# Performance work log

Measured on AMD Instinct MI355X. Metric: run time of the kernel, lower is better.

## Reference

```python
import jax, jax.numpy as jnp
import numpy as np

B, C, H, W = 8, 64, 256, 256
N_HEADS = 4
MODES_X, MODES_Y = 32, 32 // 2 + 1  # rfft half-spectrum along last dim
O_PER_HEAD = C // N_HEADS


def setup_inputs() -> dict:
    key = jax.random.key(0)
    k1, k2, k3 = jax.random.split(key, 3)
    x = jax.random.normal(k1, (B, C, H, W), dtype=jnp.float32)
    weights_real = jax.random.normal(k2, (N_HEADS, C, O_PER_HEAD, MODES_X, MODES_Y), dtype=jnp.float32) * 0.01
    weights_imag = jax.random.normal(k3, (N_HEADS, C, O_PER_HEAD, MODES_X, MODES_Y), dtype=jnp.float32) * 0.01
    bias = jnp.zeros((C, 1, 1), dtype=jnp.float32)
    return {"x": x, "weights_real": weights_real, "weights_imag": weights_imag, "bias": bias}


def reference(x, weights_real, weights_imag, bias):
    b, c, h, w = x.shape
    nh, _, o, mxw, myw = weights_real.shape
    # rfft2 with ortho norm, matching torch.fft.rfft2(..., norm='ortho')
    xf = jnp.fft.rfft2(x, norm="ortho")  # [B, C, H, W//2+1] complex64
    fH, fW = xf.shape[-2], xf.shape[-1]
    mx = min(mxw, fH)
    my = min(myw, fW)
    wgt = weights_real[..., :mx, :my] + 1j * weights_imag[..., :mx, :my]  # [nh, C, o, mx, my]
    # all heads at once: torch loop 'biXY,ioXY->boXY' per head == 'bixy,hioxy->bhoxy'
    prod = jnp.einsum("bixy,hioxy->bhoxy", xf[:, :, :mx, :my], wgt)  # [B, nh, o, mx, my]
    out_f = jnp.zeros((b, nh, o, fH, fW), dtype=prod.dtype).at[..., :mx, :my].set(prod)
    out = jnp.fft.irfft2(out_f, s=(h, w), norm="ortho")  # [B, nh, o, H, W] real
    # torch.cat over heads along channel dim == head-major reshape
    out = out.reshape(b, nh * o, h, w)
    return out + bias  # bias [C,1,1] broadcasts
```

## Files before the change

kernel.cpp:

```cpp
#include <hip/hip_runtime.h>
#include <hip/hip_bf16.h>

#define NROWS 131072
#define MY 17
#define MX 32


#define K1_ROWS 30
#define NCHUNK 9

__global__ __launch_bounds__(512) void f1_fw(const float* __restrict__ x,
                                             float2* __restrict__ X2) {
    __shared__ __align__(16) float s_lds[4][K1_ROWS][68];
    __shared__ float2 xs[4352];
    int t = threadIdx.x;
    int bc = blockIdx.x;
    const float* xp = x + (long)bc * 65536;

    int j = t % 17;
    int r = t / 17;
    int rc = r < K1_ROWS ? r : 0;
    int odd = j & 1;
    float ca = odd ? 0.f : ((j & 2) ? -1.f : 1.f);
    float cb = odd ? (((j & 3) == 1) ? -1.f : 1.f) : 0.f;
    float cj, sj;
    sincospif((float)j * (1.0f / 128.0f), &sj, &cj);
    sj = -sj;
    float swv, cwv;
    sincospif((float)j * 0.25f, &swv, &cwv);
    swv = -swv;
    float k1c = cwv * ca - swv * cb;
    float k2c = swv * ca + cwv * cb;
    const float4* A4 = (const float4*)&s_lds[odd ? 1 : 0][rc][0];
    const float4* B4 = (const float4*)&s_lds[odd ? 3 : 2][rc][0];

    float4 q0, q1, q2, q3;

#define F1_REGLOAD(cc)                                                         \
    {                                                                          \
        int nr_ = ((cc) < 8) ? K1_ROWS : 16;                                   \
        int items_ = nr_ * 16;                                                 \
        int it = t < items_ ? t : items_ - 1;                                  \
        int rr = it >> 4, cq = it & 15;                                        \
        const float4* xr =                                                     \
            (const float4*)(xp + ((cc) * K1_ROWS + rr) * 256) + cq;            \
        q0 = xr[0];                                                            \
        q1 = xr[16];                                                           \
        q2 = xr[32];                                                           \
        q3 = xr[48];                                                           \
    }

    F1_REGLOAD(0)

    for (int c = 0; c < NCHUNK; ++c) {
        int nr = (c < 8) ? K1_ROWS : 16;
        int items = nr * 16;

        if (t < items) {
            int rr = t >> 4, cq = t & 15;
            float4 s02p, s02m, s13p, s13m;
            s02p.x = q0.x + q2.x; s02p.y = q0.y + q2.y;
            s02p.z = q0.z + q2.z; s02p.w = q0.w + q2.w;
            s02m.x = q0.x - q2.x; s02m.y = q0.y - q2.y;
            s02m.z = q0.z - q2.z; s02m.w = q0.w - q2.w;
            s13p.x = q1.x + q3.x; s13p.y = q1.y + q3.y;
            s13p.z = q1.z + q3.z; s13p.w = q1.w + q3.w;
            s13m.x = q1.x - q3.x; s13m.y = q1.y - q3.y;
            s13m.z = q1.z - q3.z; s13m.w = q1.w - q3.w;
            *(float4*)&s_lds[0][rr][cq * 4] = s02p;
            *(float4*)&s_lds[1][rr][cq * 4] = s02m;
            *(float4*)&s_lds[2][rr][cq * 4] = s13p;
            *(float4*)&s_lds[3][rr][cq * 4] = s13m;
        }
        __syncthreads();

        if (c + 1 < NCHUNK) F1_REGLOAD(c + 1)

        if (t < 510 && r < nr) {
            float pc = 1.f, ps = 0.f;
            float ar0 = 0, ai0 = 0;

#define K1_STEP(a0e, b0e, a0f, b0f)                                   \
  { float t0re = fmaf(k1c, (b0f), fmaf(cwv, (a0f), fmaf(ca, (b0e), (a0e)))); \
    float t0im = fmaf(k2c, (b0f), fmaf(swv, (a0f), cb * (b0e)));      \
    ar0 = fmaf(t0re, pc, ar0); ar0 = fmaf(-t0im, ps, ar0);            \
    ai0 = fmaf(t0re, ps, ai0); ai0 = fmaf(t0im, pc, ai0);             \
    float nps = fmaf(pc, sj, ps * cj);                                \
    pc = fmaf(pc, cj, -(ps * sj)); ps = nps; }

#pragma unroll 2
            for (int l4 = 0; l4 < 8; ++l4) {
                float4 va0 = A4[l4], vb0 = B4[l4];
                float4 vA0 = A4[8 + l4], vB0 = B4[8 + l4];
                K1_STEP(va0.x, vb0.x, vA0.x, vB0.x)
                K1_STEP(va0.y, vb0.y, vA0.y, vB0.y)
                K1_STEP(va0.z, vb0.z, vA0.z, vB0.z)
                K1_STEP(va0.w, vb0.w, vA0.w, vB0.w)
            }
#undef K1_STEP

            int h = c * K1_ROWS + r;
            xs[h * 17 + j] = make_float2(ar0, ai0);
        }
        __syncthreads();
    }

    for (int q = t; q < 2176; q += 512) {
        float2 a = xs[q], b = xs[q + 2176];
        xs[q] = make_float2(a.x + b.x, a.y + b.y);
        xs[q + 2176] = make_float2(a.x - b.x, a.y - b.y);
    }
    __syncthreads();

    for (int q = t; q < 544; q += 512) {
        int kx = q / 17, ky = q % 17;
        int kodd = kx & 1;
        float cA = kodd ? 0.f : ((kx & 2) ? -1.f : 1.f);
        float cB = kodd ? (((kx & 3) == 1) ? -1.f : 1.f) : 0.f;
        float cBn = -cB;
        const float2* Aq = xs + (kodd ? 2176 : 0) + ky;
        float cs, ss;
        sincospif((float)kx * (1.0f / 128.0f), &ss, &cs);
        ss = -ss;
        float pc = 1.f, psn = 0.f;
        float ar = 0.f, ai = 0.f;
#pragma unroll 4
        for (int m = 0; m < 64; ++m) {
            float2 a = Aq[m * 17];
            float2 b = Aq[1088 + m * 17];
            float yre = fmaf(cBn, b.y, fmaf(cA, b.x, a.x));
            float yim = fmaf(cB, b.x, fmaf(cA, b.y, a.y));
            ar = fmaf(yre, pc, ar); ar = fmaf(-yim, psn, ar);
            ai = fmaf(yre, psn, ai); ai = fmaf(yim, pc, ai);
            float npc = pc * cs - psn * ss;
            psn = pc * ss + psn * cs;
            pc = npc;
        }
        X2[(long)bc * 544 + q] = make_float2(ar, ai);
    }
#undef F1_REGLOAD
}

__global__ __launch_bounds__(512) void k_ab(const float2* __restrict__ X2,
                                            const float* __restrict__ wr_g,
                                            const float* __restrict__ wi_g,
                                            float2* __restrict__ Z) {
    __shared__ float2 psh[544];
    int t = threadIdx.x;
    int plane = blockIdx.x;
    int b = plane >> 6;
    int ho = plane & 63;
    int n = ho >> 4;
    int o = ho & 15;

    for (int q = t; q < 544; q += 512) {
        const float2* xp = X2 + (long)b * 64 * 544 + q;
        const float* wrp = wr_g + ((long)(n * 64) * 16 + o) * 544 + q;
        const float* wip = wi_g + ((long)(n * 64) * 16 + o) * 544 + q;
        float ar = 0.f, ai = 0.f;
#pragma unroll 4
        for (int i = 0; i < 64; ++i) {
            float2 xv = xp[i * 544];
            float wvr = wrp[i * 8704];
            float wvi = wip[i * 8704];
            ar += xv.x * wvr - xv.y * wvi;
            ai += xv.x * wvi + xv.y * wvr;
        }
        psh[q] = make_float2(ar, ai);
    }
    __syncthreads();

    {
        int h = t & 255;
        int half = t >> 8;
        int kyb = half ? 9 : 0;
        int cnt = half ? 8 : 9;
        float chh, shh;
        sincospif((float)h * (1.0f / 128.0f), &shh, &chh);
        float pc = 1.f, psn = 0.f;
        float ar[9], ai[9];
#pragma unroll
        for (int u = 0; u < 9; ++u) { ar[u] = 0.f; ai[u] = 0.f; }

        const float2* pq = psh + kyb;
        for (int kx = 0; kx < 32; ++kx) {
#pragma unroll
            for (int u = 0; u < 9; ++u) {
                if (u < cnt) {
                    float2 v = pq[kx * 17 + u];
                    ar[u] += v.x * pc - v.y * psn;
                    ai[u] += v.x * psn + v.y * pc;
                }
            }
            float npc = pc * chh - psn * shh;
            psn = pc * shh + psn * chh;
            pc = npc;
        }
        float2* zp = Z + (long)plane * 4352 + h;
#pragma unroll
        for (int u = 0; u < 9; ++u)
            if (u < cnt) zp[(kyb + u) * 256] = make_float2(ar[u], ai[u]);
    }
}

__global__ __launch_bounds__(256) void k_c(const float2* __restrict__ Z,
                                           const float* __restrict__ bias,
                                           float* __restrict__ out) {
    __shared__ float2 zsl[544];
    int t = threadIdx.x;
    int bi = blockIdx.x;
    int plane = bi >> 3;
    int base = (bi & 7) * 32;
    const float2* zp = Z + (long)plane * 4352;

    for (int q = t; q < 544; q += 256) {
        int ky = q >> 5, r = q & 31;
        zsl[r * 17 + ky] = zp[ky * 256 + base + r];
    }
    __syncthreads();

    int wv = t >> 6;
    int lane = t & 63;
    float bv = bias[plane & 63];
    float c0, s0;
    sincospif((float)lane * (1.0f / 128.0f), &s0, &c0);
    const float inv = 1.0f / 65536.0f;
    const float inv2 = 2.0f / 65536.0f;
    long ob_plane = (long)plane * 65536 + (long)base * 256;

    for (int it = 0; it < 4; ++it) {
        int r0 = it * 8 + wv * 2;
        float pc = c0, psn = s0;
        float a00 = 0, a01 = 0, a02 = 0, a03 = 0;
        float a10 = 0, a11 = 0, a12 = 0, a13 = 0;

#pragma unroll
        for (int ky = 1; ky <= 16; ++ky) {
            float2 z0 = zsl[r0 * 17 + ky];
            float2 z1 = zsl[(r0 + 1) * 17 + ky];
            float A0 = z0.x * pc - z0.y * psn;
            float B0 = z0.x * psn + z0.y * pc;
            float A1 = z1.x * pc - z1.y * psn;
            float B1 = z1.x * psn + z1.y * pc;
            a00 += A0; a10 += A1;
            a01 += ((ky & 3) == 0) ? A0 : ((ky & 3) == 1) ? -B0 : ((ky & 3) == 2) ? -A0 : B0;
            a11 += ((ky & 3) == 0) ? A1 : ((ky & 3) == 1) ? -B1 : ((ky & 3) == 2) ? -A1 : B1;
            a02 += (ky & 1) ? -A0 : A0;
            a12 += (ky & 1) ? -A1 : A1;
            a03 += ((ky & 3) == 0) ? A0 : ((ky & 3) == 1) ? B0 : ((ky & 3) == 2) ? -A0 : -B0;
            a13 += ((ky & 3) == 0) ? A1 : ((ky & 3) == 1) ? B1 : ((ky & 3) == 2) ? -A1 : -B1;
            float npc = pc * c0 - psn * s0;
            psn = pc * s0 + psn * c0;
            pc = npc;
        }
        float base0 = zsl[r0 * 17].x * inv + bv;
        float base1 = zsl[(r0 + 1) * 17].x * inv + bv;
        long ob0 = ob_plane + (long)r0 * 256;
        long ob1 = ob0 + 256;
        out[ob0 + lane]       = fmaf(a00, inv2, base0);
        out[ob0 + 64 + lane]  = fmaf(a01, inv2, base0);
        out[ob0 + 128 + lane] = fmaf(a02, inv2, base0);
        out[ob0 + 192 + lane] = fmaf(a03, inv2, base0);
        out[ob1 + lane]       = fmaf(a10, inv2, base1);
        out[ob1 + 64 + lane]  = fmaf(a11, inv2, base1);
        out[ob1 + 128 + lane] = fmaf(a12, inv2, base1);
        out[ob1 + 192 + lane] = fmaf(a13, inv2, base1);
    }
}

extern "C" void kernel_launch(void* const* d_in, const int* in_sizes, int n_in,
                              void* d_out, int out_size, void* d_ws, size_t ws_size,
                              hipStream_t stream) {
    const float* x = (const float*)d_in[0];
    const float* wr = (const float*)d_in[1];
    const float* wi = (const float*)d_in[2];
    const float* bias = (const float*)d_in[3];
    float* out = (float*)d_out;
    float* ws = (float*)d_ws;

    float2* Z  = (float2*)(ws + 512);
    float2* X2 = (float2*)(ws + 4456960);

    hipLaunchKernelGGL(f1_fw, dim3(512), dim3(512), 0, stream, x, X2);
    hipLaunchKernelGGL(k_ab, dim3(512), dim3(512), 0, stream, X2, wr, wi, Z);
    hipLaunchKernelGGL(k_c, dim3(4096), dim3(256), 0, stream, Z, bias, out);
}
```

Baseline: 127.1 us.

## Fold upper-half frequencies into lower half and read Z directly in k_c

The final inverse-transform kernel no longer stages Z through LDS with a barrier. Each wave reads its rows' frequency coefficients straight from global memory through uniform loads. It also pre-combines bins ky and ky+8 using a per-lane twiddle exp(i*pi*lane/16), exploiting the output periodicity, which halves the length of the inner twiddle-rotation loop. This trades the shared-memory load and sync for more global reads and extra registers per thread.

```diff
diff --git a/kernel.cpp b/kernel.cpp
--- a/kernel.cpp
+++ b/kernel.cpp
@@ -206,42 +206,52 @@
 __global__ __launch_bounds__(256) void k_c(const float2* __restrict__ Z,
                                            const float* __restrict__ bias,
                                            float* __restrict__ out) {
-    __shared__ float2 zsl[544];
     int t = threadIdx.x;
     int bi = blockIdx.x;
     int plane = bi >> 3;
     int base = (bi & 7) * 32;
-    const float2* zp = Z + (long)plane * 4352;
-
-    for (int q = t; q < 544; q += 256) {
-        int ky = q >> 5, r = q & 31;
-        zsl[r * 17 + ky] = zp[ky * 256 + base + r];
-    }
-    __syncthreads();
-
-    int wv = t >> 6;
+    int wv = __builtin_amdgcn_readfirstlane(t >> 6);
     int lane = t & 63;
     float bv = bias[plane & 63];
+
     float c0, s0;
     sincospif((float)lane * (1.0f / 128.0f), &s0, &c0);
+    float c8, s8;
+    sincospif((float)lane * (1.0f / 16.0f), &s8, &c8);
+
+    const float2* zp = Z + (long)plane * 4352 + base;
     const float inv = 1.0f / 65536.0f;
     const float inv2 = 2.0f / 65536.0f;
     long ob_plane = (long)plane * 65536 + (long)base * 256;
 
     for (int it = 0; it < 4; ++it) {
         int r0 = it * 8 + wv * 2;
+        const float2* zr0 = zp + r0;
+        const float2* zr1 = zp + r0 + 1;
+
+        float dc0 = zr0[0].x, dc1 = zr1[0].x;
+        float zz0r[9], zz0i[9], zz1r[9], zz1i[9];
+#pragma unroll
+        for (int ky = 1; ky <= 8; ++ky) {
+            float2 a0 = zr0[ky * 256], b0 = zr0[(ky + 8) * 256];
+            float2 a1 = zr1[ky * 256], b1 = zr1[(ky + 8) * 256];
+            zz0r[ky - 1] = fmaf(b0.x, c8, fmaf(-b0.y, s8, a0.x));
+            zz0i[ky - 1] = fmaf(b0.x, s8, fmaf(b0.y, c8, a0.y));
+            zz1r[ky - 1] = fmaf(b1.x, c8, fmaf(-b1.y, s8, a1.x));
+            zz1i[ky - 1] = fmaf(b1.x, s8, fmaf(b1.y, c8, a1.y));
+        }
+
         float pc = c0, psn = s0;
         float a00 = 0, a01 = 0, a02 = 0, a03 = 0;
         float a10 = 0, a11 = 0, a12 = 0, a13 = 0;
-
-#pragma unroll
-        for (int ky = 1; ky <= 16; ++ky) {
-            float2 z0 = zsl[r0 * 17 + ky];
-            float2 z1 = zsl[(r0 + 1) * 17 + ky];
-            float A0 = z0.x * pc - z0.y * psn;
-            float B0 = z0.x * psn + z0.y * pc;
-            float A1 = z1.x * pc - z1.y * psn;
-            float B1 = z1.x * psn + z1.y * pc;
+#pragma unroll
+        for (int ky = 1; ky <= 8; ++ky) {
+            float zr0v = zz0r[ky - 1], zi0v = zz0i[ky - 1];
+            float zr1v = zz1r[ky - 1], zi1v = zz1i[ky - 1];
+            float A0 = zr0v * pc - zi0v * psn;
+            float B0 = zr0v * psn + zi0v * pc;
+            float A1 = zr1v * pc - zi1v * psn;
+            float B1 = zr1v * psn + zi1v * pc;
             a00 += A0; a10 += A1;
             a01 += ((ky & 3) == 0) ? A0 : ((ky & 3) == 1) ? -B0 : ((ky & 3) == 2) ? -A0 : B0;
             a11 += ((ky & 3) == 0) ? A1 : ((ky & 3) == 1) ? -B1 : ((ky & 3) == 2) ? -A1 : B1;
@@ -253,8 +263,8 @@
             psn = pc * s0 + psn * c0;
             pc = npc;
         }
-        float base0 = zsl[r0 * 17].x * inv + bv;
-        float base1 = zsl[(r0 + 1) * 17].x * inv + bv;
+        float base0 = dc0 * inv + bv;
+        float base1 = dc1 * inv + bv;
         long ob0 = ob_plane + (long)r0 * 256;
         long ob1 = ob0 + 256;
         out[ob0 + lane]       = fmaf(a00, inv2, base0);
```

Measured after the change: 132.4 us. 4.2% more time.
